# Kernel optimization log

Measured on AMD Instinct MI355X. Metric: run time of the kernel, lower is better.

Reference implementation:

```python
import jax, jax.numpy as jnp
import numpy as np

B, C, H, W = 8, 192, 128, 128
HEADS = 16
EPS = 1e-12  # F.normalize eps


def setup_inputs() -> dict:
    key = jax.random.key(0)
    k1, k2, k3, k4 = jax.random.split(key, 4)
    s = 0.02
    return {
        "x": jax.random.normal(k1, (B, C, H, W), dtype=jnp.float32),
        "w_qkv": jax.random.normal(k2, (3 * C, C), dtype=jnp.float32) * s,
        "w_dw": jax.random.normal(k3, (C, 1, 3, 3), dtype=jnp.float32) * s,
        "w_proj": jax.random.normal(k4, (C, C), dtype=jnp.float32) * s,
        "temperature": jnp.ones((HEADS, 1, 1), dtype=jnp.float32),
    }


def reference(x, w_qkv, w_dw, w_proj, temperature):
    b, c, h, w = x.shape
    heads = HEADS
    hd = c // heads  # per-head channel dim
    hw = h * w

    # 1x1 conv qkv projection: [b, 3c, h, w]
    qkv = jnp.einsum('bchw,oc->bohw', x, w_qkv)
    q, k, v = jnp.split(qkv, 3, axis=1)

    def to_heads(t):
        return t.reshape(b, heads, hd, hw)  # b head c (h w)

    q, k, v = to_heads(q), to_heads(k), to_heads(v)

    # L2-normalize along spatial dim (matches F.normalize with eps clamp)
    q = q / jnp.maximum(jnp.linalg.norm(q, axis=-1, keepdims=True), EPS)
    k = k / jnp.maximum(jnp.linalg.norm(k, axis=-1, keepdims=True), EPS)

    # channel-wise attention: [b, head, hd, hd]
    attn = jnp.einsum('bhcn,bhdn->bhcd', q, k) * temperature
    attn = jax.nn.softmax(attn, axis=-1)

    out = jnp.einsum('bhcd,bhdn->bhcn', attn, v)  # [b, head, hd, hw]
    out = out.reshape(b, c, h, w)

    # depthwise 3x3 conv, padding=1
    out = jax.lax.conv_general_dilated(
        out, w_dw, window_strides=(1, 1), padding=((1, 1), (1, 1)),
        dimension_numbers=('NCHW', 'OIHW', 'NCHW'), feature_group_count=c)

    # 1x1 conv projection
    out = jnp.einsum('bchw,oc->bohw', out, w_proj)
    return out
```

## Files before the change

### kernel.cpp

```cpp
#include <hip/hip_runtime.h>

#define B_   8
#define C_   192
#define HW_  16384
#define W_   128
#define NH_  16
#define HD_  12

#define OFF_G      0u
#define OFF_WQKV   1179648u
#define OFF_WDW    1622016u
#define OFF_TEMP   1628928u
#define OFF_WPROJ  1629184u
#define OFF_M      1702912u
#define OFF_Y      2292736u

typedef __attribute__((ext_vector_type(8))) __bf16 bf16x8;
typedef __attribute__((ext_vector_type(8))) short  short8;
typedef __attribute__((ext_vector_type(4))) short  short4v;
typedef __attribute__((ext_vector_type(4))) float  floatx4;

__device__ __forceinline__ unsigned short f2bfu(float f) {
  union { float f; unsigned u; } v; v.f = f;
  unsigned r = (v.u + 0x7FFFu + ((v.u >> 16) & 1u)) >> 16;
  return (unsigned short)r;
}
__device__ __forceinline__ float bfu2f(unsigned short h) {
  union { unsigned u; float f; } v; v.u = ((unsigned)h) << 16;
  return v.f;
}
__device__ __forceinline__ bool bfmode(const void* temp) {
  return ((const unsigned*)temp)[0] != 0x3F800000u;
}
__device__ __forceinline__ float in_ld(const void* p, int i, bool bf) {
  return bf ? bfu2f(((const unsigned short*)p)[i]) : ((const float*)p)[i];
}
__device__ __forceinline__ floatx4 mfma16(short8 a, short8 b, floatx4 c) {
  union U { short8 s; bf16x8 b; } ua, ub;
  ua.s = a; ub.s = b;
  return __builtin_amdgcn_mfma_f32_16x16x32_bf16(ua.b, ub.b, c, 0, 0, 0);
}
__device__ __forceinline__ short8 row_frag(const void* x, bool bf, long elemoff) {
  short8 r;
  if (bf) {
    r = *(const short8*)((const unsigned short*)x + elemoff);
  } else {
    const float4* p4 = (const float4*)((const float*)x + elemoff);
    float4 a = p4[0], b = p4[1];
    r[0] = (short)f2bfu(a.x); r[1] = (short)f2bfu(a.y);
    r[2] = (short)f2bfu(a.z); r[3] = (short)f2bfu(a.w);
    r[4] = (short)f2bfu(b.x); r[5] = (short)f2bfu(b.y);
    r[6] = (short)f2bfu(b.z); r[7] = (short)f2bfu(b.w);
  }
  return r;
}

__global__ __launch_bounds__(256) void k_init(const void* wqkv, const void* wdw,
                                              const void* wproj, const void* temp,
                                              unsigned char* ws) {
  bool bf = bfmode(temp);
  int idx = blockIdx.x * 256 + threadIdx.x;
  if (idx < 294912) { ((float*)(ws + OFF_G))[idx] = 0.f; return; }
  int i = idx - 294912;
  if (i < 110592) { ((float*)(ws + OFF_WQKV))[i] = in_ld(wqkv, i, bf); return; }
  i -= 110592;
  if (i < 1728) { ((float*)(ws + OFF_WDW))[i] = in_ld(wdw, i, bf); return; }
  i -= 1728;
  if (i < 16) { ((float*)(ws + OFF_TEMP))[i] = in_ld(temp, i, bf); return; }
  i -= 16;
  if (i < 36864) {
    unsigned short* wp = (unsigned short*)(ws + OFF_WPROJ);
    wp[i] = bf ? ((const unsigned short*)wproj)[i] : f2bfu(((const float*)wproj)[i]);
  }
}

__global__ __launch_bounds__(256) void k_gram(const void* x, const void* temp,
                                              unsigned char* ws) {
  bool bf = bfmode(temp);
  float* G = (float*)(ws + OFF_G);
  int b = blockIdx.x >> 5, grp = blockIdx.x & 31;
  int tid = threadIdx.x;
  int w = tid >> 6, lane = tid & 63, m = lane & 15, q = lane >> 4;
  long xb = (long)b * C_ * HW_;
  __shared__ __align__(16) short xs[C_][136];
  floatx4 acc[3][12];
  floatx4 zz = {0.f, 0.f, 0.f, 0.f};
  for (int i = 0; i < 3; ++i)
    for (int t = 0; t < 12; ++t) acc[i][t] = zz;
  for (int sl = 0; sl < 4; ++sl) {
    int px0 = (grp * 4 + sl) * 128;
    if (sl) __syncthreads();
    for (int i = 0; i < 12; ++i) {
      int chunk = i * 256 + tid;
      int c = chunk >> 4, p8 = chunk & 15;
      short8 v = row_frag(x, bf, xb + (long)c * HW_ + px0 + p8 * 8);
      *(short8*)&xs[c][p8 * 8] = v;
    }
    __syncthreads();
    for (int ks = 0; ks < 4; ++ks) {
      int col = ks * 32 + q * 8;
      short8 A0 = *(const short8*)&xs[(3 * w + 0) * 16 + m][col];
      short8 A1 = *(const short8*)&xs[(3 * w + 1) * 16 + m][col];
      short8 A2 = *(const short8*)&xs[(3 * w + 2) * 16 + m][col];
      for (int t = 0; t < 12; ++t) {
        short8 F = *(const short8*)&xs[t * 16 + m][col];
        acc[0][t] = mfma16(A0, F, acc[0][t]);
        acc[1][t] = mfma16(A1, F, acc[1][t]);
        acc[2][t] = mfma16(A2, F, acc[2][t]);
      }
    }
  }
  for (int i = 0; i < 3; ++i)
    for (int t = 0; t < 12; ++t)
      for (int r = 0; r < 4; ++r)
        atomicAdd(&G[((long)b * C_ + (3 * w + i) * 16 + q * 4 + r) * C_ + t * 16 + m],
                  acc[i][t][r]);
}

__global__ __launch_bounds__(256) void k_attn(unsigned char* ws) {
  int b = blockIdx.x >> 4, h = blockIdx.x & 15;
  int tid = threadIdx.x;
  const float* G  = (const float*)(ws + OFF_G) + (long)b * C_ * C_;
  const float* Wf = (const float*)(ws + OFF_WQKV);
  const float* Wq = Wf + (h * HD_) * C_;
  const float* Wk = Wf + (C_ + h * HD_) * C_;
  const float* Wv = Wf + (2 * C_ + h * HD_) * C_;
  float tmprt = ((const float*)(ws + OFF_TEMP))[h];
  unsigned short* Mh = (unsigned short*)(ws + OFF_M) + ((long)b * C_ + h * HD_) * C_;

  __shared__ float Gs[32][C_ + 1];
  __shared__ float tq[HD_][C_], tk[HD_][C_];
  __shared__ float Sm[HD_][HD_], Aw[HD_][HD_], nq[HD_], nk[HD_];

  for (int jblk = 0; jblk < 6; ++jblk) {
    for (int i = tid; i < 32 * C_; i += 256) {
      int jj = i / C_, a = i - jj * C_;
      Gs[jj][a] = G[(jblk * 32 + jj) * C_ + a];
    }
    __syncthreads();
    for (int i = tid; i < 2 * HD_ * 32; i += 256) {
      int jj = i & 31, rest = i >> 5;
      int c = rest % HD_, which = rest / HD_;
      const float* Wrow = (which ? Wk : Wq) + c * C_;
      float s = 0.f;
      for (int a = 0; a < C_; ++a) s += Wrow[a] * Gs[jj][a];
      float (*dst)[C_] = which ? tk : tq;
      dst[c][jblk * 32 + jj] = s;
    }
    __syncthreads();
  }
  if (tid < 144) {
    int c = tid / HD_, d = tid - c * HD_;
    float s = 0.f;
    for (int a = 0; a < C_; ++a) s += tq[c][a] * Wk[d * C_ + a];
    Sm[c][d] = s;
  } else if (tid < 156) {
    int c = tid - 144; float s = 0.f;
    for (int a = 0; a < C_; ++a) s += tq[c][a] * Wq[c * C_ + a];
    nq[c] = s;
  } else if (tid < 168) {
    int c = tid - 156; float s = 0.f;
    for (int a = 0; a < C_; ++a) s += tk[c][a] * Wk[c * C_ + a];
    nk[c] = s;
  }
  __syncthreads();
  if (tid < HD_) {
    int c = tid;
    float qn = fmaxf(sqrtf(fmaxf(nq[c], 0.f)), 1e-12f);
    float L[HD_], mx = -1e30f;
    for (int d = 0; d < HD_; ++d) {
      float kn = fmaxf(sqrtf(fmaxf(nk[d], 0.f)), 1e-12f);
      L[d] = Sm[c][d] / (qn * kn) * tmprt;
      mx = fmaxf(mx, L[d]);
    }
    float ssum = 0.f;
    for (int d = 0; d < HD_; ++d) { L[d] = __expf(L[d] - mx); ssum += L[d]; }
    float inv = 1.f / ssum;
    for (int d = 0; d < HD_; ++d) Aw[c][d] = L[d] * inv;
  }
  __syncthreads();
  for (int i = tid; i < HD_ * C_; i += 256) {
    int c = i / C_, j = i - c * C_;
    float s = 0.f;
    for (int d = 0; d < HD_; ++d) s += Aw[c][d] * Wv[d * C_ + j];
    Mh[c * C_ + j] = f2bfu(s);
  }
}

__global__ __launch_bounds__(256) void k_mx(const void* x, const void* temp,
                                            unsigned char* ws) {
  bool bf = bfmode(temp);
  const unsigned short* Mb = (const unsigned short*)(ws + OFF_M);
  unsigned short* y = (unsigned short*)(ws + OFF_Y);
  int b = blockIdx.x >> 7, px0 = (blockIdx.x & 127) * 128;
  int tid = threadIdx.x;
  int w = tid >> 6, lane = tid & 63, m = lane & 15, q = lane >> 4;
  long xb = (long)b * C_ * HW_;
  __shared__ __align__(16) short xsT[128][200];
  for (int i = 0; i < 3; ++i) {
    int chunk = i * 256 + tid;
    int p8 = chunk & 15, cq = chunk >> 4;
    short8 r0 = row_frag(x, bf, xb + (long)(cq * 4 + 0) * HW_ + px0 + p8 * 8);
    short8 r1 = row_frag(x, bf, xb + (long)(cq * 4 + 1) * HW_ + px0 + p8 * 8);
    short8 r2 = row_frag(x, bf, xb + (long)(cq * 4 + 2) * HW_ + px0 + p8 * 8);
    short8 r3 = row_frag(x, bf, xb + (long)(cq * 4 + 3) * HW_ + px0 + p8 * 8);
    for (int j = 0; j < 8; ++j) {
      short4v v = { r0[j], r1[j], r2[j], r3[j] };
      *(short4v*)&xsT[p8 * 8 + j][cq * 4] = v;
    }
  }
  __syncthreads();
  floatx4 acc[3][8];
  floatx4 zz = {0.f, 0.f, 0.f, 0.f};
  for (int i = 0; i < 3; ++i)
    for (int pt = 0; pt < 8; ++pt) acc[i][pt] = zz;
  for (int k = 0; k < 6; ++k) {
    int c0 = k * 32;
    const unsigned short* Mrow = Mb + (long)b * C_ * C_ + c0 + q * 8;
    short8 A0 = *(const short8*)(Mrow + ((3 * w + 0) * 16 + m) * C_);
    short8 A1 = *(const short8*)(Mrow + ((3 * w + 1) * 16 + m) * C_);
    short8 A2 = *(const short8*)(Mrow + ((3 * w + 2) * 16 + m) * C_);
    for (int pt = 0; pt < 8; ++pt) {
      short8 Bf = *(const short8*)&xsT[pt * 16 + m][c0 + q * 8];
      acc[0][pt] = mfma16(A0, Bf, acc[0][pt]);
      acc[1][pt] = mfma16(A1, Bf, acc[1][pt]);
      acc[2][pt] = mfma16(A2, Bf, acc[2][pt]);
    }
  }
  for (int i = 0; i < 3; ++i) {
    int rowb = (3 * w + i) * 16 + q * 4;
    for (int pt = 0; pt < 8; ++pt) {
      int px = px0 + pt * 16 + m;
      for (int rg = 0; rg < 4; ++rg)
        y[((long)b * C_ + rowb + rg) * HW_ + px] = f2bfu(acc[i][pt][rg]);
    }
  }
}

__global__ __launch_bounds__(256) void k_out(const void* temp, unsigned char* ws,
                                             void* out) {
  bool bf = bfmode(temp);
  const unsigned short* y = (const unsigned short*)(ws + OFF_Y);
  const float* wdw = (const float*)(ws + OFF_WDW);
  const unsigned short* Wp = (const unsigned short*)(ws + OFF_WPROJ);
  int b = blockIdx.x >> 7, irow = blockIdx.x & 127;
  int tid = threadIdx.x;
  __shared__ unsigned short dT[C_][130];
  {
    int oct = tid & 15, cq = tid >> 4;
    int p0 = oct * 8;
    for (int c = cq; c < C_; c += 16) {
      float wv[9];
      for (int t = 0; t < 9; ++t) wv[t] = wdw[c * 9 + t];
      float a0[8];
      for (int i = 0; i < 8; ++i) a0[i] = 0.f;
      const unsigned short* yc = y + ((long)b * C_ + c) * HW_;
      for (int dy = 0; dy < 3; ++dy) {
        int rr = irow + dy - 1;
        if (rr < 0 || rr > 127) continue;
        const unsigned short* yr = yc + rr * W_;
        float v[10];
        v[0] = (p0 == 0) ? 0.f : bfu2f(yr[p0 - 1]);
        union { uint4 u; unsigned short s[8]; } uu;
        uu.u = *(const uint4*)(yr + p0);
        for (int i = 0; i < 8; ++i) v[1 + i] = bfu2f(uu.s[i]);
        v[9] = (p0 + 8 >= W_) ? 0.f : bfu2f(yr[p0 + 8]);
        for (int dx = 0; dx < 3; ++dx) {
          float wc = wv[dy * 3 + dx];
          for (int i = 0; i < 8; ++i) a0[i] += wc * v[i + dx];
        }
      }
      for (int i = 0; i < 8; ++i) dT[c][p0 + i] = f2bfu(a0[i]);
    }
  }
  __syncthreads();
  int wave = tid >> 6, lane = tid & 63;
  int m = lane & 15, q = lane >> 4;
  floatx4 acc[12][2];
  floatx4 zz = {0.f, 0.f, 0.f, 0.f};
  for (int r = 0; r < 12; ++r) { acc[r][0] = zz; acc[r][1] = zz; }
  int pA = wave * 32 + m, pB = pA + 16;
  for (int k = 0; k < 6; ++k) {
    int c0 = k * 32 + q * 8;
    short8 B0, B1;
    for (int j = 0; j < 8; ++j) {
      B0[j] = (short)dT[c0 + j][pA];
      B1[j] = (short)dT[c0 + j][pB];
    }
    for (int r = 0; r < 12; ++r) {
      short8 A = *(const short8*)(Wp + (r * 16 + m) * C_ + c0);
      acc[r][0] = mfma16(A, B0, acc[r][0]);
      acc[r][1] = mfma16(A, B1, acc[r][1]);
    }
  }
  long ob = (long)b * C_ * HW_ + irow * W_;
  for (int r = 0; r < 12; ++r) {
    int o = r * 16 + q * 4;
    for (int rg = 0; rg < 4; ++rg) {
      long off = ob + (long)(o + rg) * HW_;
      float v0 = acc[r][0][rg], v1 = acc[r][1][rg];
      if (bf) {
        ((unsigned short*)out)[off + pA] = f2bfu(v0);
        ((unsigned short*)out)[off + pB] = f2bfu(v1);
      } else {
        ((float*)out)[off + pA] = v0;
        ((float*)out)[off + pB] = v1;
      }
    }
  }
}

extern "C" void kernel_launch(void* const* d_in, const int* in_sizes, int n_in,
                              void* d_out, int out_size, void* d_ws, size_t ws_size,
                              hipStream_t stream) {
  const void* x     = d_in[0];
  const void* wqkv  = d_in[1];
  const void* wdw   = d_in[2];
  const void* wproj = d_in[3];
  const void* temp  = d_in[4];
  unsigned char* ws = (unsigned char*)d_ws;
  k_init<<<dim3(1735), dim3(256), 0, stream>>>(wqkv, wdw, wproj, temp, ws);
  k_gram<<<dim3(256), dim3(256), 0, stream>>>(x, temp, ws);
  k_attn<<<dim3(128), dim3(256), 0, stream>>>(ws);
  k_mx<<<dim3(1024), dim3(256), 0, stream>>>(x, temp, ws);
  k_out<<<dim3(1024), dim3(256), 0, stream>>>(temp, ws, d_out);
}
```

Measured before the change: 400.8 us.

## Chunk depthwise-conv into MFMA projection in k_out with swizzled LDS and more waves

```diff
diff --git a/kernel.cpp b/kernel.cpp
--- a/kernel.cpp
+++ b/kernel.cpp
@@ -78,7 +78,7 @@
                                               unsigned char* ws) {
   bool bf = bfmode(temp);
   float* G = (float*)(ws + OFF_G);
-  int b = blockIdx.x >> 5, grp = blockIdx.x & 31;
+  int b = blockIdx.x >> 6, grp = blockIdx.x & 63;
   int tid = threadIdx.x;
   int w = tid >> 6, lane = tid & 63, m = lane & 15, q = lane >> 4;
   long xb = (long)b * C_ * HW_;
@@ -87,8 +87,8 @@
   floatx4 zz = {0.f, 0.f, 0.f, 0.f};
   for (int i = 0; i < 3; ++i)
     for (int t = 0; t < 12; ++t) acc[i][t] = zz;
-  for (int sl = 0; sl < 4; ++sl) {
-    int px0 = (grp * 4 + sl) * 128;
+  for (int sl = 0; sl < 2; ++sl) {
+    int px0 = (grp * 2 + sl) * 128;
     if (sl) __syncthreads();
     for (int i = 0; i < 12; ++i) {
       int chunk = i * 256 + tid;
@@ -237,7 +237,7 @@
   }
 }
 
-__global__ __launch_bounds__(256) void k_out(const void* temp, unsigned char* ws,
+__global__ __launch_bounds__(512) void k_out(const void* temp, unsigned char* ws,
                                              void* out) {
   bool bf = bfmode(temp);
   const unsigned short* y = (const unsigned short*)(ws + OFF_Y);
@@ -245,16 +245,35 @@
   const unsigned short* Wp = (const unsigned short*)(ws + OFF_WPROJ);
   int b = blockIdx.x >> 7, irow = blockIdx.x & 127;
   int tid = threadIdx.x;
-  __shared__ unsigned short dT[C_][130];
-  {
-    int oct = tid & 15, cq = tid >> 4;
-    int p0 = oct * 8;
-    for (int c = cq; c < C_; c += 16) {
-      float wv[9];
-      for (int t = 0; t < 9; ++t) wv[t] = wdw[c * 9 + t];
-      float a0[8];
-      for (int i = 0; i < 8; ++i) a0[i] = 0.f;
+  __shared__ __align__(16) unsigned dly[128 * 36];
+
+  int wv = tid >> 6, lane = tid & 63, m = lane & 15, q = lane >> 4;
+  int wr = wv >> 2, wc = wv & 3;
+  int pA = wc * 32 + m, pB = pA + 16;
+  int swzA = (pA >> 3) & 7, swzB = (pB >> 3) & 7;
+
+  int oct = tid & 15, cg = tid >> 4;
+  int p0 = oct * 8;
+  int wbase = p0 * 36 + ((((cg >> 2) ^ (oct & 7)) << 2) | (cg & 3));
+
+  floatx4 acc[6][2];
+  floatx4 zz = {0.f, 0.f, 0.f, 0.f};
+#pragma unroll
+  for (int r = 0; r < 6; ++r) { acc[r][0] = zz; acc[r][1] = zz; }
+
+  for (int ch = 0; ch < 3; ++ch) {
+    if (ch) __syncthreads();
+    float a0[8], a1[8];
+#pragma unroll
+    for (int i = 0; i < 8; ++i) { a0[i] = 0.f; a1[i] = 0.f; }
+#pragma unroll
+    for (int j = 0; j < 2; ++j) {
+      float* aj = j ? a1 : a0;
+      int c = ch * 64 + cg * 2 + j;
       const unsigned short* yc = y + ((long)b * C_ + c) * HW_;
+      float wv9[9];
+#pragma unroll
+      for (int t = 0; t < 9; ++t) wv9[t] = wdw[c * 9 + t];
       for (int dy = 0; dy < 3; ++dy) {
         int rr = irow + dy - 1;
         if (rr < 0 || rr > 127) continue;
@@ -263,39 +282,42 @@
         v[0] = (p0 == 0) ? 0.f : bfu2f(yr[p0 - 1]);
         union { uint4 u; unsigned short s[8]; } uu;
         uu.u = *(const uint4*)(yr + p0);
+#pragma unroll
         for (int i = 0; i < 8; ++i) v[1 + i] = bfu2f(uu.s[i]);
         v[9] = (p0 + 8 >= W_) ? 0.f : bfu2f(yr[p0 + 8]);
+#pragma unroll
         for (int dx = 0; dx < 3; ++dx) {
-          float wc = wv[dy * 3 + dx];
-          for (int i = 0; i < 8; ++i) a0[i] += wc * v[i + dx];
+          float wc9 = wv9[dy * 3 + dx];
+#pragma unroll
+          for (int i = 0; i < 8; ++i) aj[i] += wc9 * v[i + dx];
         }
       }
-      for (int i = 0; i < 8; ++i) dT[c][p0 + i] = f2bfu(a0[i]);
-    }
-  }
-  __syncthreads();
-  int wave = tid >> 6, lane = tid & 63;
-  int m = lane & 15, q = lane >> 4;
-  floatx4 acc[12][2];
-  floatx4 zz = {0.f, 0.f, 0.f, 0.f};
-  for (int r = 0; r < 12; ++r) { acc[r][0] = zz; acc[r][1] = zz; }
-  int pA = wave * 32 + m, pB = pA + 16;
-  for (int k = 0; k < 6; ++k) {
-    int c0 = k * 32 + q * 8;
-    short8 B0, B1;
-    for (int j = 0; j < 8; ++j) {
-      B0[j] = (short)dT[c0 + j][pA];
-      B1[j] = (short)dT[c0 + j][pB];
-    }
-    for (int r = 0; r < 12; ++r) {
-      short8 A = *(const short8*)(Wp + (r * 16 + m) * C_ + c0);
-      acc[r][0] = mfma16(A, B0, acc[r][0]);
-      acc[r][1] = mfma16(A, B1, acc[r][1]);
+    }
+#pragma unroll
+    for (int i = 0; i < 8; ++i) {
+      unsigned pk = (unsigned)f2bfu(a0[i]) | ((unsigned)f2bfu(a1[i]) << 16);
+      dly[wbase + i * 36] = pk;
+    }
+    __syncthreads();
+#pragma unroll
+    for (int ks = 0; ks < 2; ++ks) {
+      int kb = ks * 4 + q;
+      short8 B0 = *(const short8*)&dly[pA * 36 + ((kb ^ swzA) << 2)];
+      short8 B1 = *(const short8*)&dly[pB * 36 + ((kb ^ swzB) << 2)];
+      int c0 = ch * 64 + ks * 32 + q * 8;
+#pragma unroll
+      for (int r = 0; r < 6; ++r) {
+        short8 A = *(const short8*)(Wp + (wr * 96 + r * 16 + m) * C_ + c0);
+        acc[r][0] = mfma16(A, B0, acc[r][0]);
+        acc[r][1] = mfma16(A, B1, acc[r][1]);
+      }
     }
   }
   long ob = (long)b * C_ * HW_ + irow * W_;
-  for (int r = 0; r < 12; ++r) {
-    int o = r * 16 + q * 4;
+#pragma unroll
+  for (int r = 0; r < 6; ++r) {
+    int o = wr * 96 + r * 16 + q * 4;
+#pragma unroll
     for (int rg = 0; rg < 4; ++rg) {
       long off = ob + (long)(o + rg) * HW_;
       float v0 = acc[r][0][rg], v1 = acc[r][1][rg];
@@ -320,8 +342,8 @@
   const void* temp  = d_in[4];
   unsigned char* ws = (unsigned char*)d_ws;
   k_init<<<dim3(1735), dim3(256), 0, stream>>>(wqkv, wdw, wproj, temp, ws);
-  k_gram<<<dim3(256), dim3(256), 0, stream>>>(x, temp, ws);
+  k_gram<<<dim3(512), dim3(256), 0, stream>>>(x, temp, ws);
   k_attn<<<dim3(128), dim3(256), 0, stream>>>(ws);
   k_mx<<<dim3(1024), dim3(256), 0, stream>>>(x, temp, ws);
-  k_out<<<dim3(1024), dim3(256), 0, stream>>>(temp, ws, d_out);
-}
+  k_out<<<dim3(1024), dim3(512), 0, stream>>>(temp, ws, d_out);
+}
```

After: 399.5 us. No clear change (-0.3%).
